# Performance work log

Hardware: AMD Instinct MI355X
Metric: run time of the kernel (lower is better)

The kernel has to match this reference:

```python
import jax, jax.numpy as jnp
import numpy as np

N, F_IN, F_OUT, K, B = 4096, 64, 64, 5, 8
NAN_FRAC = 0.1


def ex_relu(mean, var):
    # E[ReLU(X)] for X ~ N(mean, var); where var==0 this is relu(mean).
    std = jnp.sqrt(jnp.maximum(var, 0.0))
    safe_std = jnp.where(std > 0, std, 1.0)
    z = mean / safe_std
    pdf = jnp.exp(-0.5 * z * z) / jnp.sqrt(2.0 * jnp.pi)
    cdf = 0.5 * (1.0 + jax.lax.erf(z / jnp.sqrt(2.0)))
    ex = mean * cdf + std * pdf
    return jnp.where(std > 0, ex, jnp.maximum(mean, 0.0))


def setup_inputs() -> dict:
    key = jax.random.key(0)
    ks = jax.random.split(key, 8)
    shift = jax.random.normal(ks[0], (N, N), dtype=jnp.float32) / jnp.sqrt(N)
    A2 = jax.random.uniform(ks[1], (N, N), dtype=jnp.float32) / N
    features = jax.random.normal(ks[2], (B, N, F_IN), dtype=jnp.float32)
    nan_mask = jax.random.bernoulli(ks[3], NAN_FRAC, (B, N, F_IN))
    features = jnp.where(nan_mask, jnp.nan, features)
    weight = jax.random.normal(ks[4], (F_IN, F_OUT), dtype=jnp.float32) * jnp.sqrt(2.0 / (F_IN + F_OUT))
    pi = jax.nn.log_softmax(jax.random.normal(ks[5], (K,), dtype=jnp.float32))
    mu = jax.random.normal(ks[6], (K, F_IN), dtype=jnp.float32)
    sigma = jax.random.normal(ks[7], (K, F_IN), dtype=jnp.float32) * 0.1  # log diag covariances
    return {"shift": shift, "A2": A2, "features": features,
            "weight": weight, "pi": pi, "mu": mu, "sigma": sigma}


def reference(shift, A2, features, weight, pi, mu, sigma):
    var = jnp.exp(sigma)                                    # [K,F]
    isnan = jnp.isnan(features)[:, None]                    # [B,1,N,F]
    feat_b = jnp.where(jnp.isnan(features), 0.0, features)[:, None]  # NaN-sanitized [B,1,N,F]
    mean_mat = jnp.where(isnan, mu[None, :, None, :], feat_b)        # [B,K,N,F]
    var_mat = jnp.where(isnan, var[None, :, None, :], 0.0)           # [B,K,N,F]
    # masked feature transform
    tx = jnp.einsum('bknf,fo->bkno', mean_mat, weight)       # [B,K,N,O]
    tc = jnp.einsum('bknf,fo->bkno', var_mat, weight * weight)
    # per-component graph conv (spmm)
    cx = jnp.einsum('nm,bkmo->bkno', shift, tx)
    cc = jnp.einsum('nm,bkmo->bkno', A2, tc)
    ex = ex_relu(cx, cc)                                     # [B,K,N,O]
    # responsibilities
    f_dim = features.shape[-1]
    log_n = (-0.5 * jnp.sum((mean_mat - mu[None, :, None, :]) ** 2 / var[None, :, None, :], axis=-1)
             - 0.5 * f_dim * jnp.log(2.0 * jnp.pi) - 0.5 * jnp.sum(sigma))  # [B,K,N]
    gamma = jax.nn.softmax(pi[None, :, None] + log_n, axis=1)               # softmax over components
    return jnp.sum(ex * gamma[..., None], axis=1)            # [B,N,O]
```

## Files before the change

kernel.cpp:

```cpp
#include <hip/hip_runtime.h>

#define NN 4096
#define FF 64
#define OO 64
#define KK 5
#define BB 8

typedef unsigned short bf16_t;
typedef __attribute__((ext_vector_type(8))) short short8;
typedef __attribute__((ext_vector_type(4))) float floatx4;

__device__ __forceinline__ unsigned short f2bf(float x) {
  unsigned int u = __float_as_uint(x);
  return (unsigned short)((u + 0x7fffu + ((u >> 16) & 1u)) >> 16);
}
__device__ __forceinline__ float bf2f(unsigned short h) {
  return __uint_as_float(((unsigned int)h) << 16);
}
__device__ __forceinline__ bool is_nan(float x) {
  return (__float_as_uint(x) & 0x7fffffffu) > 0x7f800000u;
}
__device__ __forceinline__ void gld16(const void* g, void* l) {
  __builtin_amdgcn_global_load_lds(
      (__attribute__((address_space(1))) const unsigned int*)g,
      (__attribute__((address_space(3))) unsigned int*)l, 16, 0, 0);
}

union S8 { short8 s; int4 i; uint4 u; };

__device__ __forceinline__ short8 addbf(short8 x, short8 y) {
  S8 a, b, r;
  a.s = x; b.s = y;
#pragma unroll
  for (int e = 0; e < 8; ++e)
    r.s[e] = (short)f2bf(bf2f((unsigned short)a.s[e]) + bf2f((unsigned short)b.s[e]));
  return r.s;
}

__global__ __launch_bounds__(256) void prep_kernel(
    const float* __restrict__ W, const float* __restrict__ sigma, const float* __restrict__ mu,
    float* __restrict__ ivarr, bf16_t* __restrict__ WTb,
    bf16_t* __restrict__ EkT, bf16_t* __restrict__ DkT) {
  int t = blockIdx.x * 256 + threadIdx.x;
  if (t < KK * FF) ivarr[t] = expf(-sigma[t]);
  if (t < FF * OO) {
    int o = t >> 6, f = t & 63;
    WTb[t] = f2bf(W[f * OO + o]);
  }
  int k = t >> 12, o = (t >> 6) & 63, f = t & 63;
  if (k < KK) {
    float w = W[f * OO + o];
    EkT[t] = f2bf(mu[k * FF + f] * w);
    DkT[t] = f2bf(expf(sigma[k * FF + f]) * w * w);
  }
}

__global__ __launch_bounds__(256) void cast2_kernel(
    const float* __restrict__ s0, const float* __restrict__ s1,
    bf16_t* __restrict__ d0, bf16_t* __restrict__ d1) {
  int i = (blockIdx.x * 256 + threadIdx.x) * 8;
  if (i + 8 > NN * NN) return;
  float4 a = *(const float4*)(s0 + i);
  float4 b = *(const float4*)(s0 + i + 4);
  union { unsigned short h[8]; uint4 v; } r;
  r.h[0] = f2bf(a.x); r.h[1] = f2bf(a.y); r.h[2] = f2bf(a.z); r.h[3] = f2bf(a.w);
  r.h[4] = f2bf(b.x); r.h[5] = f2bf(b.y); r.h[6] = f2bf(b.z); r.h[7] = f2bf(b.w);
  *(uint4*)(d0 + i) = r.v;
  a = *(const float4*)(s1 + i);
  b = *(const float4*)(s1 + i + 4);
  r.h[0] = f2bf(a.x); r.h[1] = f2bf(a.y); r.h[2] = f2bf(a.z); r.h[3] = f2bf(a.w);
  r.h[4] = f2bf(b.x); r.h[5] = f2bf(b.y); r.h[6] = f2bf(b.z); r.h[7] = f2bf(b.w);
  *(uint4*)(d1 + i) = r.v;
}

__global__ __launch_bounds__(256) void stage1_kernel(
    const float* __restrict__ feat, const float* __restrict__ pi,
    const float* __restrict__ mu, const float* __restrict__ ivarr,
    bf16_t* __restrict__ BigBT, float* __restrict__ gamma) {
  __shared__ bf16_t F0s[64][66];
  __shared__ bf16_t Ms[64][66];
  int t = threadIdx.x;
  int b = blockIdx.x >> 6;
  int n0 = (blockIdx.x & 63) << 6;
  int r = t >> 2, c4 = t & 3;
  const float* frow = feat + ((size_t)b * NN + n0 + r) * FF + c4 * 16;

  float s[KK] = {0.f, 0.f, 0.f, 0.f, 0.f};
#pragma unroll
  for (int ch = 0; ch < 4; ++ch) {
    float4 v4 = *(const float4*)(frow + ch * 4);
    float vv[4] = {v4.x, v4.y, v4.z, v4.w};
#pragma unroll
    for (int e = 0; e < 4; ++e) {
      int f = c4 * 16 + ch * 4 + e;
      bool nb = is_nan(vv[e]);
      float x = nb ? 0.f : vv[e];
      F0s[r][f] = nb ? (bf16_t)0 : f2bf(x);
      Ms[r][f] = nb ? (bf16_t)0x3F80 : (bf16_t)0;
#pragma unroll
      for (int k = 0; k < KK; ++k) {
        float d = nb ? 0.f : (x - mu[k * FF + f]);
        s[k] = fmaf(d * d, ivarr[k * FF + f], s[k]);
      }
    }
  }
#pragma unroll
  for (int k = 0; k < KK; ++k) {
    s[k] += __shfl_xor(s[k], 1);
    s[k] += __shfl_xor(s[k], 2);
  }
  if (c4 == 0) {
    float l[KK], mx = -3.0e38f;
#pragma unroll
    for (int k = 0; k < KK; ++k) { l[k] = pi[k] - 0.5f * s[k]; mx = fmaxf(mx, l[k]); }
    float ek[KK], sum = 0.f;
#pragma unroll
    for (int k = 0; k < KK; ++k) { ek[k] = expf(l[k] - mx); sum += ek[k]; }
    float inv = 1.0f / sum;
#pragma unroll
    for (int k = 0; k < KK; ++k)
      gamma[((size_t)(b * KK + k)) * NN + n0 + r] = ek[k] * inv;
  }
  __syncthreads();
#pragma unroll
  for (int it = 0; it < 2; ++it) {
    int f = it * 32 + (t >> 3);
    int nc = t & 7;
    union { bf16_t h[8]; uint4 v; } p;
#pragma unroll
    for (int e = 0; e < 8; ++e) p.h[e] = F0s[nc * 8 + e][f];
    *(uint4*)(BigBT + ((size_t)(b * 128 + f)) * NN + n0 + nc * 8) = p.v;
#pragma unroll
    for (int e = 0; e < 8; ++e) p.h[e] = Ms[nc * 8 + e][f];
    *(uint4*)(BigBT + ((size_t)(b * 128 + 64 + f)) * NN + n0 + nc * 8) = p.v;
  }
}

__global__ __launch_bounds__(256) void gemm_bt_kernel(
    const bf16_t* __restrict__ A0, const bf16_t* __restrict__ BigBT, bf16_t* __restrict__ C0,
    const bf16_t* __restrict__ A1, bf16_t* __restrict__ C1) {
  __shared__ bf16_t As[128 * 64];
  __shared__ bf16_t Bs[128 * 64];
  int bid = blockIdx.x;
  const bf16_t* A;
  bf16_t* C;
  int tile_m, tile_c, kh, Cld;
  bool isP;
  if (bid < 512) {
    isP = false; A = A0;
    kh = bid & 1; int tmp = bid >> 1;
    tile_m = tmp >> 3; tile_c = tmp & 7; Cld = 1024;
    C = C0 + (size_t)kh * (NN * 1024);
  } else {
    isP = true; A = A1;
    int b2 = bid - 512;
    kh = b2 & 1; int tmp = b2 >> 1;
    tile_m = tmp >> 2; tile_c = tmp & 3; Cld = 512;
    C = C1 + (size_t)kh * (NN * 512);
  }

  int tid = threadIdx.x;
  int wave = tid >> 6, lane = tid & 63;
  int wm = wave >> 1, wc = wave & 1;

  int srow = wave * 32 + (lane >> 3);
  int scol = (((lane & 7) ^ (lane >> 3)) << 3);
  const bf16_t* Ag = A + (size_t)(tile_m * 128 + srow) * NN + scol;
  int browi;
  if (!isP) {
    browi = tile_c * 128 + srow;
  } else {
    int c2 = tile_c * 128 + srow;
    browi = ((c2 >> 6) << 7) + 64 + (c2 & 63);
  }
  const bf16_t* Bg = BigBT + (size_t)browi * NN + scol;
  bf16_t* AsW = &As[(wave * 32) * 64];
  bf16_t* BsW = &Bs[(wave * 32) * 64];

  floatx4 acc[4][4];
#pragma unroll
  for (int i = 0; i < 4; ++i)
#pragma unroll
    for (int j = 0; j < 4; ++j) acc[i][j] = (floatx4){0.f, 0.f, 0.f, 0.f};

  int ml = lane & 15;
  int q = lane >> 4;
  int sw = ml & 7;

#pragma unroll 1
  for (int kt = kh * 32; kt < kh * 32 + 32; ++kt) {
    int k0 = kt * 64;
    __syncthreads();
#pragma unroll
    for (int i = 0; i < 4; ++i) {
      gld16(Ag + (size_t)(i * 8) * NN + k0, AsW + (i * 8) * 64);
      gld16(Bg + (size_t)(i * 8) * NN + k0, BsW + (i * 8) * 64);
    }
    __syncthreads();
#pragma unroll
    for (int ks = 0; ks < 2; ++ks) {
      int chunk = (((ks * 4 + q) ^ sw) << 3);
      short8 a[4], bb[4];
#pragma unroll
      for (int i = 0; i < 4; ++i)
        a[i] = *(const short8*)&As[(wm * 64 + i * 16 + ml) * 64 + chunk];
#pragma unroll
      for (int j = 0; j < 4; ++j)
        bb[j] = *(const short8*)&Bs[(wc * 64 + j * 16 + ml) * 64 + chunk];
#pragma unroll
      for (int i = 0; i < 4; ++i)
#pragma unroll
        for (int j = 0; j < 4; ++j)
          acc[i][j] = __builtin_amdgcn_mfma_f32_16x16x32_bf16(a[i], bb[j], acc[i][j], 0, 0, 0);
    }
  }

  int colb = tile_c * 128 + wc * 64 + ml;
#pragma unroll
  for (int i = 0; i < 4; ++i) {
    int mrow = tile_m * 128 + wm * 64 + i * 16 + q * 4;
#pragma unroll
    for (int j = 0; j < 4; ++j)
#pragma unroll
      for (int r = 0; r < 4; ++r)
        C[(size_t)(mrow + r) * Cld + colb + j * 16] = f2bf(acc[i][j][r]);
  }
}

__global__ __launch_bounds__(256) void stage2_kernel(
    const bf16_t* __restrict__ QRp, const bf16_t* __restrict__ Pp,
    const bf16_t* __restrict__ WTb, const bf16_t* __restrict__ EkT,
    const bf16_t* __restrict__ DkT, const float* __restrict__ gamma,
    float* __restrict__ out) {
  const bf16_t* QR1 = QRp + (size_t)NN * 1024;
  const bf16_t* Pp1 = Pp + (size_t)NN * 512;
  int t = threadIdx.x;
  int b = blockIdx.x >> 6;
  int n0 = (blockIdx.x & 63) << 6;
  int w = t >> 6, lane = t & 63, m = lane & 15, q = lane >> 4;
  int n = n0 + w * 16 + m;

  short8 Qf[2], Rf[2], Pf[2], wfr[4][2];
#pragma unroll
  for (int ks = 0; ks < 2; ++ks) {
    size_t oq = (size_t)n * 1024 + b * 128 + ks * 32 + q * 8;
    size_t op = (size_t)n * 512 + b * 64 + ks * 32 + q * 8;
    Qf[ks] = addbf(*(const short8*)(QRp + oq), *(const short8*)(QR1 + oq));
    Rf[ks] = addbf(*(const short8*)(QRp + oq + 64), *(const short8*)(QR1 + oq + 64));
    Pf[ks] = addbf(*(const short8*)(Pp + op), *(const short8*)(Pp1 + op));
  }
#pragma unroll
  for (int ot = 0; ot < 4; ++ot)
#pragma unroll
    for (int ks = 0; ks < 2; ++ks)
      wfr[ot][ks] = *(const short8*)(WTb + (ot * 16 + m) * 64 + ks * 32 + q * 8);

  floatx4 z = (floatx4){0.f, 0.f, 0.f, 0.f};
  floatx4 QW[4], osum[4];
#pragma unroll
  for (int ot = 0; ot < 4; ++ot) {
    QW[ot] = __builtin_amdgcn_mfma_f32_16x16x32_bf16(Qf[0], wfr[ot][0], z, 0, 0, 0);
    QW[ot] = __builtin_amdgcn_mfma_f32_16x16x32_bf16(Qf[1], wfr[ot][1], QW[ot], 0, 0, 0);
    osum[ot] = z;
  }

#pragma unroll
  for (int k = 0; k < KK; ++k) {
    float4 g4 = *(const float4*)(gamma + ((size_t)(b * KK + k)) * NN + n0 + w * 16 + q * 4);
    float gg[4] = {g4.x, g4.y, g4.z, g4.w};
#pragma unroll
    for (int ot = 0; ot < 4; ++ot) {
      const bf16_t* ek = EkT + ((k * 64 + ot * 16 + m) * 64) + q * 8;
      const bf16_t* dk = DkT + ((k * 64 + ot * 16 + m) * 64) + q * 8;
      short8 e0 = *(const short8*)ek, e1 = *(const short8*)(ek + 32);
      short8 d0 = *(const short8*)dk, d1 = *(const short8*)(dk + 32);
      floatx4 cx4 = __builtin_amdgcn_mfma_f32_16x16x32_bf16(Rf[0], e0, QW[ot], 0, 0, 0);
      cx4 = __builtin_amdgcn_mfma_f32_16x16x32_bf16(Rf[1], e1, cx4, 0, 0, 0);
      floatx4 cc4 = __builtin_amdgcn_mfma_f32_16x16x32_bf16(Pf[0], d0, z, 0, 0, 0);
      cc4 = __builtin_amdgcn_mfma_f32_16x16x32_bf16(Pf[1], d1, cc4, 0, 0, 0);
#pragma unroll
      for (int r = 0; r < 4; ++r) {
        float mm = cx4[r];
        float v = cc4[r];
        float sd = sqrtf(fmaxf(v, 0.f));
        float zz = mm / (sd > 0.f ? sd : 1.f);
        float pdf = expf(-0.5f * zz * zz) * 0.3989422804014327f;
        float cdf = 0.5f * (1.f + erff(zz * 0.7071067811865476f));
        float ex = sd > 0.f ? fmaf(mm, cdf, sd * pdf) : fmaxf(mm, 0.f);
        osum[ot][r] = fmaf(gg[r], ex, osum[ot][r]);
      }
    }
  }

#pragma unroll
  for (int ot = 0; ot < 4; ++ot)
#pragma unroll
    for (int r = 0; r < 4; ++r)
      out[((size_t)b * NN + n0 + w * 16 + q * 4 + r) * OO + ot * 16 + m] = osum[ot][r];
}

extern "C" void kernel_launch(void* const* d_in, const int* in_sizes, int n_in,
                              void* d_out, int out_size, void* d_ws, size_t ws_size,
                              hipStream_t stream) {
  const float* shift = (const float*)d_in[0];
  const float* A2    = (const float*)d_in[1];
  const float* feat  = (const float*)d_in[2];
  const float* W     = (const float*)d_in[3];
  const float* pi    = (const float*)d_in[4];
  const float* mu    = (const float*)d_in[5];
  const float* sigma = (const float*)d_in[6];
  float* out = (float*)d_out;

  char* ws = (char*)d_ws;
  bf16_t* shift_bf = (bf16_t*)(ws + 0);
  bf16_t* A2_bf    = (bf16_t*)(ws + 33554432);
  bf16_t* BigBT    = (bf16_t*)(ws + 67108864);
  bf16_t* QRp      = (bf16_t*)(ws + 75497472);
  bf16_t* Pp       = (bf16_t*)(ws + 92274688);
  float*  gam      = (float*) (ws + 100663296);
  float*  ivarr    = (float*) (ws + 101318656);
  bf16_t* WTb      = (bf16_t*)(ws + 101319936);
  bf16_t* EkT      = (bf16_t*)(ws + 101328128);
  bf16_t* DkT      = (bf16_t*)(ws + 101369088);

  prep_kernel<<<80, 256, 0, stream>>>(W, sigma, mu, ivarr, WTb, EkT, DkT);
  cast2_kernel<<<8192, 256, 0, stream>>>(shift, A2, shift_bf, A2_bf);
  stage1_kernel<<<512, 256, 0, stream>>>(feat, pi, mu, ivarr, BigBT, gam);
  gemm_bt_kernel<<<768, 256, 0, stream>>>(shift_bf, BigBT, QRp, A2_bf, Pp);
  stage2_kernel<<<512, 256, 0, stream>>>(QRp, Pp, WTb, EkT, DkT, gam, out);
}
```

Baseline: 285.3 us.

## Fuse prep, cast and stage1 into one front kernel; remap GEMM block order

Merges the three preparatory launches (weight prep, fp32-to-bf16 cast of the two NxN matrices, and feature sanitisation plus responsibilities) into one kernel that dispatches on block index. The ivar buffer goes away and expf(-sigma) is recomputed inline in stage1. The GEMM block index mapping is also changed so consecutive blocks share A-row tiles and the two K-halves interleave, which should improve L2 reuse. This removes two launch gaps at the cost of redundant exp work and a heavier shared-memory footprint for the cast blocks, which may lower their occupancy.

```diff
diff --git a/kernel.cpp b/kernel.cpp
--- a/kernel.cpp
+++ b/kernel.cpp
@@ -37,51 +37,53 @@
   return r.s;
 }
 
-__global__ __launch_bounds__(256) void prep_kernel(
-    const float* __restrict__ W, const float* __restrict__ sigma, const float* __restrict__ mu,
-    float* __restrict__ ivarr, bf16_t* __restrict__ WTb,
-    bf16_t* __restrict__ EkT, bf16_t* __restrict__ DkT) {
-  int t = blockIdx.x * 256 + threadIdx.x;
-  if (t < KK * FF) ivarr[t] = expf(-sigma[t]);
-  if (t < FF * OO) {
-    int o = t >> 6, f = t & 63;
-    WTb[t] = f2bf(W[f * OO + o]);
-  }
-  int k = t >> 12, o = (t >> 6) & 63, f = t & 63;
-  if (k < KK) {
-    float w = W[f * OO + o];
-    EkT[t] = f2bf(mu[k * FF + f] * w);
-    DkT[t] = f2bf(expf(sigma[k * FF + f]) * w * w);
-  }
-}
-
-__global__ __launch_bounds__(256) void cast2_kernel(
-    const float* __restrict__ s0, const float* __restrict__ s1,
-    bf16_t* __restrict__ d0, bf16_t* __restrict__ d1) {
-  int i = (blockIdx.x * 256 + threadIdx.x) * 8;
-  if (i + 8 > NN * NN) return;
-  float4 a = *(const float4*)(s0 + i);
-  float4 b = *(const float4*)(s0 + i + 4);
-  union { unsigned short h[8]; uint4 v; } r;
-  r.h[0] = f2bf(a.x); r.h[1] = f2bf(a.y); r.h[2] = f2bf(a.z); r.h[3] = f2bf(a.w);
-  r.h[4] = f2bf(b.x); r.h[5] = f2bf(b.y); r.h[6] = f2bf(b.z); r.h[7] = f2bf(b.w);
-  *(uint4*)(d0 + i) = r.v;
-  a = *(const float4*)(s1 + i);
-  b = *(const float4*)(s1 + i + 4);
-  r.h[0] = f2bf(a.x); r.h[1] = f2bf(a.y); r.h[2] = f2bf(a.z); r.h[3] = f2bf(a.w);
-  r.h[4] = f2bf(b.x); r.h[5] = f2bf(b.y); r.h[6] = f2bf(b.z); r.h[7] = f2bf(b.w);
-  *(uint4*)(d1 + i) = r.v;
-}
-
-__global__ __launch_bounds__(256) void stage1_kernel(
-    const float* __restrict__ feat, const float* __restrict__ pi,
-    const float* __restrict__ mu, const float* __restrict__ ivarr,
-    bf16_t* __restrict__ BigBT, float* __restrict__ gamma) {
+__global__ __launch_bounds__(256) void front_kernel(
+    const float* __restrict__ shift, const float* __restrict__ A2,
+    const float* __restrict__ feat, const float* __restrict__ W,
+    const float* __restrict__ pi, const float* __restrict__ mu,
+    const float* __restrict__ sigma,
+    bf16_t* __restrict__ shift_bf, bf16_t* __restrict__ A2_bf,
+    bf16_t* __restrict__ BigBT, float* __restrict__ gamma,
+    bf16_t* __restrict__ WTb, bf16_t* __restrict__ EkT, bf16_t* __restrict__ DkT) {
   __shared__ bf16_t F0s[64][66];
   __shared__ bf16_t Ms[64][66];
+  int bb = blockIdx.x;
+
+  if (bb < 8192) {
+    int i = (bb * 256 + threadIdx.x) * 8;
+    float4 a = *(const float4*)(shift + i);
+    float4 b = *(const float4*)(shift + i + 4);
+    union { unsigned short h[8]; uint4 v; } r;
+    r.h[0] = f2bf(a.x); r.h[1] = f2bf(a.y); r.h[2] = f2bf(a.z); r.h[3] = f2bf(a.w);
+    r.h[4] = f2bf(b.x); r.h[5] = f2bf(b.y); r.h[6] = f2bf(b.z); r.h[7] = f2bf(b.w);
+    *(uint4*)(shift_bf + i) = r.v;
+    a = *(const float4*)(A2 + i);
+    b = *(const float4*)(A2 + i + 4);
+    r.h[0] = f2bf(a.x); r.h[1] = f2bf(a.y); r.h[2] = f2bf(a.z); r.h[3] = f2bf(a.w);
+    r.h[4] = f2bf(b.x); r.h[5] = f2bf(b.y); r.h[6] = f2bf(b.z); r.h[7] = f2bf(b.w);
+    *(uint4*)(A2_bf + i) = r.v;
+    return;
+  }
+
+  if (bb >= 8704) {
+    int t = (bb - 8704) * 256 + threadIdx.x;
+    if (t < FF * OO) {
+      int o = t >> 6, f = t & 63;
+      WTb[t] = f2bf(W[f * OO + o]);
+    }
+    int k = t >> 12, o = (t >> 6) & 63, f = t & 63;
+    if (k < KK) {
+      float w = W[f * OO + o];
+      EkT[t] = f2bf(mu[k * FF + f] * w);
+      DkT[t] = f2bf(expf(sigma[k * FF + f]) * w * w);
+    }
+    return;
+  }
+
+  int blk = bb - 8192;
   int t = threadIdx.x;
-  int b = blockIdx.x >> 6;
-  int n0 = (blockIdx.x & 63) << 6;
+  int b = blk >> 6;
+  int n0 = (blk & 63) << 6;
   int r = t >> 2, c4 = t & 3;
   const float* frow = feat + ((size_t)b * NN + n0 + r) * FF + c4 * 16;
 
@@ -100,7 +102,7 @@
 #pragma unroll
       for (int k = 0; k < KK; ++k) {
         float d = nb ? 0.f : (x - mu[k * FF + f]);
-        s[k] = fmaf(d * d, ivarr[k * FF + f], s[k]);
+        s[k] = fmaf(d * d * expf(-sigma[k * FF + f]), 1.0f, s[k]);
       }
     }
   }
@@ -141,21 +143,17 @@
     const bf16_t* __restrict__ A1, bf16_t* __restrict__ C1) {
   __shared__ bf16_t As[128 * 64];
   __shared__ bf16_t Bs[128 * 64];
-  int bid = blockIdx.x;
+  int x = blockIdx.x & 7;
+  int j = blockIdx.x >> 3;
   const bf16_t* A;
   bf16_t* C;
   int tile_m, tile_c, kh, Cld;
-  bool isP;
-  if (bid < 512) {
-    isP = false; A = A0;
-    kh = bid & 1; int tmp = bid >> 1;
-    tile_m = tmp >> 3; tile_c = tmp & 7; Cld = 1024;
+  bool isP = (j >= 64);
+  if (!isP) {
+    A = A0; tile_c = x; tile_m = j >> 1; kh = j & 1; Cld = 1024;
     C = C0 + (size_t)kh * (NN * 1024);
   } else {
-    isP = true; A = A1;
-    int b2 = bid - 512;
-    kh = b2 & 1; int tmp = b2 >> 1;
-    tile_m = tmp >> 2; tile_c = tmp & 3; Cld = 512;
+    A = A1; tile_m = j - 64; tile_c = x & 3; kh = x >> 2; Cld = 512;
     C = C1 + (size_t)kh * (NN * 512);
   }
 
@@ -181,7 +179,7 @@
 #pragma unroll
   for (int i = 0; i < 4; ++i)
 #pragma unroll
-    for (int j = 0; j < 4; ++j) acc[i][j] = (floatx4){0.f, 0.f, 0.f, 0.f};
+    for (int j2 = 0; j2 < 4; ++j2) acc[i][j2] = (floatx4){0.f, 0.f, 0.f, 0.f};
 
   int ml = lane & 15;
   int q = lane >> 4;
@@ -205,13 +203,13 @@
       for (int i = 0; i < 4; ++i)
         a[i] = *(const short8*)&As[(wm * 64 + i * 16 + ml) * 64 + chunk];
 #pragma unroll
-      for (int j = 0; j < 4; ++j)
-        bb[j] = *(const short8*)&Bs[(wc * 64 + j * 16 + ml) * 64 + chunk];
+      for (int j2 = 0; j2 < 4; ++j2)
+        bb[j2] = *(const short8*)&Bs[(wc * 64 + j2 * 16 + ml) * 64 + chunk];
 #pragma unroll
       for (int i = 0; i < 4; ++i)
 #pragma unroll
-        for (int j = 0; j < 4; ++j)
-          acc[i][j] = __builtin_amdgcn_mfma_f32_16x16x32_bf16(a[i], bb[j], acc[i][j], 0, 0, 0);
+        for (int j2 = 0; j2 < 4; ++j2)
+          acc[i][j2] = __builtin_amdgcn_mfma_f32_16x16x32_bf16(a[i], bb[j2], acc[i][j2], 0, 0, 0);
     }
   }
 
@@ -220,10 +218,10 @@
   for (int i = 0; i < 4; ++i) {
     int mrow = tile_m * 128 + wm * 64 + i * 16 + q * 4;
 #pragma unroll
-    for (int j = 0; j < 4; ++j)
+    for (int j2 = 0; j2 < 4; ++j2)
 #pragma unroll
       for (int r = 0; r < 4; ++r)
-        C[(size_t)(mrow + r) * Cld + colb + j * 16] = f2bf(acc[i][j][r]);
+        C[(size_t)(mrow + r) * Cld + colb + j2 * 16] = f2bf(acc[i][j2][r]);
   }
 }
 
@@ -318,14 +316,12 @@
   bf16_t* QRp      = (bf16_t*)(ws + 75497472);
   bf16_t* Pp       = (bf16_t*)(ws + 92274688);
   float*  gam      = (float*) (ws + 100663296);
-  float*  ivarr    = (float*) (ws + 101318656);
-  bf16_t* WTb      = (bf16_t*)(ws + 101319936);
-  bf16_t* EkT      = (bf16_t*)(ws + 101328128);
-  bf16_t* DkT      = (bf16_t*)(ws + 101369088);
-
-  prep_kernel<<<80, 256, 0, stream>>>(W, sigma, mu, ivarr, WTb, EkT, DkT);
-  cast2_kernel<<<8192, 256, 0, stream>>>(shift, A2, shift_bf, A2_bf);
-  stage1_kernel<<<512, 256, 0, stream>>>(feat, pi, mu, ivarr, BigBT, gam);
+  bf16_t* WTb      = (bf16_t*)(ws + 101318656);
+  bf16_t* EkT      = (bf16_t*)(ws + 101326848);
+  bf16_t* DkT      = (bf16_t*)(ws + 101367808);
+
+  front_kernel<<<8784, 256, 0, stream>>>(shift, A2, feat, W, pi, mu, sigma,
+                                         shift_bf, A2_bf, BigBT, gam, WTb, EkT, DkT);
   gemm_bt_kernel<<<768, 256, 0, stream>>>(shift_bf, BigBT, QRp, A2_bf, Pp);
   stage2_kernel<<<512, 256, 0, stream>>>(QRp, Pp, WTb, EkT, DkT, gam, out);
 }
```

After: 295.0 us. 1.03x slower.
